# Performance work log

Measured on AMD Instinct MI355X. Metric: run time of the kernel, lower is better.

The kernel has to match this reference:

```python
import jax, jax.numpy as jnp
import numpy as np

B, L, DM = 2, 2048, 2048
DI = 2 * DM          # d_inner = expand * d_model
N = 16               # d_state
K = 4                # d_conv
R = DM // 16         # dt_rank = ceil(d_model/16) = 128
FF = 8192            # intermediate_size
EPS = 1e-5


def _silu(x):
    return x * jax.nn.sigmoid(x)


def _ln(x, w, b):
    mu = jnp.mean(x, -1, keepdims=True)
    var = jnp.mean((x - mu) ** 2, -1, keepdims=True)
    return (x - mu) * jax.lax.rsqrt(var + EPS) * w + b


def setup_inputs() -> dict:
    key = jax.random.key(0)
    ks = jax.random.split(key, 8)

    def w(k, shape, fan_in):
        return jax.random.normal(k, shape, jnp.float32) / np.sqrt(fan_in).astype(np.float32)

    return {
        "hidden_states": jax.random.normal(ks[0], (B, L, DM), jnp.float32),
        "ln1_w": jnp.ones((DM,), jnp.float32),
        "ln1_b": jnp.zeros((DM,), jnp.float32),
        "W_in": w(ks[1], (2 * DI, DM), DM),      # in_proj (x and gate merged)
        "conv_w": w(ks[2], (DI, K), K),           # depthwise causal conv weights
        "conv_b": jnp.zeros((DI,), jnp.float32),
        "W_x": w(ks[3], (R + 2 * N, DI), DI),     # x_proj -> [dt_rank | B | C]
        "W_dt": w(ks[4], (DI, R), R),             # dt_proj (bias applied in scan)
        "b_dt": jnp.full((DI,), -2.0, jnp.float32),
        "A": -jnp.tile(jnp.arange(1.0, N + 1.0, dtype=jnp.float32), (DI, 1)),  # (DI, N)
        "Dp": jnp.ones((DI,), jnp.float32),
        "W_out": w(ks[5], (DM, DI), DI),
        "ln2_w": jnp.ones((DM,), jnp.float32),
        "ln2_b": jnp.zeros((DM,), jnp.float32),
        "W_fc1": w(ks[6], (2 * FF, DM), DM),      # GLU: [gate | y]
        "W_fc2": w(ks[7], (DM, FF), FF),
    }


def reference(hidden_states, ln1_w, ln1_b, W_in, conv_w, conv_b, W_x, W_dt, b_dt,
              A, Dp, W_out, ln2_w, ln2_b, W_fc1, W_fc2):
    # --- input layernorm + Phi4Mamba (prefill path: causal_conv1d_fn + selective_scan_fn) ---
    res = hidden_states
    x = _ln(hidden_states, ln1_w, ln1_b)

    xz = jnp.einsum('bld,ed->ble', x, W_in)           # (B, L, 2*DI)
    xs, gate = jnp.split(xz, 2, axis=-1)              # each (B, L, DI)

    # depthwise causal conv1d (width K) fused with silu
    xp = jnp.pad(xs, ((0, 0), (K - 1, 0), (0, 0)))
    conv = conv_b
    for k in range(K):
        conv = conv + xp[:, k:k + L, :] * conv_w[:, k]
    xs = _silu(conv)                                  # (B, L, DI)

    ssm = jnp.einsum('bld,ed->ble', xs, W_x)          # (B, L, R+2N)
    dt, Bm, Cm = ssm[..., :R], ssm[..., R:R + N], ssm[..., R + N:]
    delta = jax.nn.softplus(jnp.einsum('blr,dr->bld', dt, W_dt) + b_dt)  # (B, L, DI)

    def step(h, inp):
        d_t, b_t, c_t, x_t = inp                       # (B,DI),(B,N),(B,N),(B,DI)
        h = jnp.exp(d_t[..., None] * A) * h + (d_t * x_t)[..., None] * b_t[:, None, :]
        return h, jnp.einsum('bdn,bn->bd', h, c_t)

    h0 = jnp.zeros((B, DI, N), xs.dtype)
    _, ys = jax.lax.scan(step, h0, (delta.transpose(1, 0, 2), Bm.transpose(1, 0, 2),
                                    Cm.transpose(1, 0, 2), xs.transpose(1, 0, 2)))
    y = ys.transpose(1, 0, 2) + Dp * xs               # (B, L, DI)
    y = y * _silu(gate)                                # selective_scan z-gating
    attn_out = jnp.einsum('bld,ed->ble', y, W_out)    # (B, L, DM)

    hs = res + attn_out

    # --- post layernorm + GLU MLP ---
    res2 = hs
    x2 = _ln(hs, ln2_w, ln2_b)
    gy = jnp.einsum('bld,ed->ble', x2, W_fc1)         # (B, L, 2*FF)
    g, yy = jnp.split(gy, 2, axis=-1)
    mlp = jnp.einsum('blf,df->bld', yy * _silu(g), W_fc2)
    return res2 + mlp
```

## Files before the change

### kernel.cpp

```cpp
#include <hip/hip_runtime.h>
#include <hip/hip_bf16.h>

typedef unsigned short u16;
typedef unsigned int u32;

#define L_SEQ 2048
#define DMODEL 2048
#define DINNER 4096
#define NSTATE 16
#define MROWS 4096
#define CHUNK 32
#define NCHK  64

typedef __bf16 bf16x8 __attribute__((ext_vector_type(8)));
typedef float f32x4 __attribute__((ext_vector_type(4)));

__device__ __forceinline__ u16 f2bf(float f) {
    union { float f; u32 u; } v; v.f = f;
    u32 u = v.u;
    u32 r = (u + 0x7fffu + ((u >> 16) & 1u)) >> 16;
    return (u16)r;
}
__device__ __forceinline__ float bf2f(u16 h) {
    union { u32 u; float f; } v; v.u = ((u32)h) << 16;
    return v.f;
}

__device__ __forceinline__ void gload16(const void* g, void* l) {
    __builtin_amdgcn_global_load_lds((const __attribute__((address_space(1))) void*)g,
                                     (__attribute__((address_space(3))) void*)l, 16, 0, 0);
}

__global__ __launch_bounds__(256) void cvt_kernel(const float* __restrict__ src,
                                                  u16* __restrict__ dst, long nsrc) {
    long i = ((long)blockIdx.x * 256 + threadIdx.x) * 8;
    union { uint4 v; u16 u[8]; } o;
    if (i < nsrc) {
        f32x4 a = *(const f32x4*)(src + i);
        f32x4 b = *(const f32x4*)(src + i + 4);
#pragma unroll
        for (int j = 0; j < 4; ++j) { o.u[j] = f2bf(a[j]); o.u[4 + j] = f2bf(b[j]); }
    } else {
#pragma unroll
        for (int j = 0; j < 8; ++j) o.u[j] = 0;
    }
    *(uint4*)(dst + i) = o.v;
}

__global__ __launch_bounds__(256) void ln_kernel(const float* __restrict__ in,
                                                 const float* __restrict__ w,
                                                 const float* __restrict__ b,
                                                 u16* __restrict__ out) {
    const long row = blockIdx.x;
    const float* x = in + row * DMODEL;
    const int t = threadIdx.x;
    f32x4 v0 = *(const f32x4*)(x + t * 8);
    f32x4 v1 = *(const f32x4*)(x + t * 8 + 4);
    float s = 0.f, sq = 0.f;
#pragma unroll
    for (int j = 0; j < 4; ++j) {
        s += v0[j] + v1[j];
        sq += v0[j] * v0[j] + v1[j] * v1[j];
    }
#pragma unroll
    for (int off = 32; off > 0; off >>= 1) {
        s += __shfl_down(s, off);
        sq += __shfl_down(sq, off);
    }
    __shared__ float red[8];
    __shared__ float stats[2];
    const int wid = t >> 6, lane = t & 63;
    if (lane == 0) { red[wid] = s; red[4 + wid] = sq; }
    __syncthreads();
    if (t == 0) {
        float S = red[0] + red[1] + red[2] + red[3];
        float Q = red[4] + red[5] + red[6] + red[7];
        float mu = S / (float)DMODEL;
        stats[0] = mu;
        stats[1] = rsqrtf(Q / (float)DMODEL - mu * mu + 1e-5f);
    }
    __syncthreads();
    float mu = stats[0], rstd = stats[1];
    union { uint4 v; u16 u[8]; } o;
#pragma unroll
    for (int j = 0; j < 8; ++j) {
        float xv = (j < 4) ? v0[j] : v1[j - 4];
        o.u[j] = f2bf((xv - mu) * rstd * w[t * 8 + j] + b[t * 8 + j]);
    }
    *(uint4*)(out + row * DMODEL + t * 8) = o.v;
}

__global__ __launch_bounds__(256) void reduce_ln_kernel(const float* __restrict__ p0,
                                                        const float* __restrict__ p1,
                                                        const float* __restrict__ add,
                                                        const float* __restrict__ w,
                                                        const float* __restrict__ b,
                                                        float* __restrict__ hs_out,
                                                        u16* __restrict__ ln_out) {
    const long row = blockIdx.x;
    const long base = row * DMODEL;
    const int t = threadIdx.x;
    f32x4 v0, v1;
    {
        f32x4 a0 = *(const f32x4*)(p0 + base + t * 8);
        f32x4 a1 = *(const f32x4*)(p0 + base + t * 8 + 4);
        f32x4 b0 = *(const f32x4*)(p1 + base + t * 8);
        f32x4 b1 = *(const f32x4*)(p1 + base + t * 8 + 4);
        f32x4 c0 = *(const f32x4*)(add + base + t * 8);
        f32x4 c1 = *(const f32x4*)(add + base + t * 8 + 4);
#pragma unroll
        for (int j = 0; j < 4; ++j) { v0[j] = a0[j] + b0[j] + c0[j]; v1[j] = a1[j] + b1[j] + c1[j]; }
    }
    *(f32x4*)(hs_out + base + t * 8) = v0;
    *(f32x4*)(hs_out + base + t * 8 + 4) = v1;
    float s = 0.f, sq = 0.f;
#pragma unroll
    for (int j = 0; j < 4; ++j) {
        s += v0[j] + v1[j];
        sq += v0[j] * v0[j] + v1[j] * v1[j];
    }
#pragma unroll
    for (int off = 32; off > 0; off >>= 1) {
        s += __shfl_down(s, off);
        sq += __shfl_down(sq, off);
    }
    __shared__ float red[8];
    __shared__ float stats[2];
    const int wid = t >> 6, lane = t & 63;
    if (lane == 0) { red[wid] = s; red[4 + wid] = sq; }
    __syncthreads();
    if (t == 0) {
        float S = red[0] + red[1] + red[2] + red[3];
        float Q = red[4] + red[5] + red[6] + red[7];
        float mu = S / (float)DMODEL;
        stats[0] = mu;
        stats[1] = rsqrtf(Q / (float)DMODEL - mu * mu + 1e-5f);
    }
    __syncthreads();
    float mu = stats[0], rstd = stats[1];
    union { uint4 v; u16 u[8]; } o;
#pragma unroll
    for (int j = 0; j < 8; ++j) {
        float xv = (j < 4) ? v0[j] : v1[j - 4];
        o.u[j] = f2bf((xv - mu) * rstd * w[t * 8 + j] + b[t * 8 + j]);
    }
    *(uint4*)(ln_out + base + t * 8) = o.v;
}

template <int MODE>
__global__ __launch_bounds__(256) void gemm_bt(const u16* __restrict__ A,
                                               const u16* __restrict__ W,
                                               float* __restrict__ Cf,
                                               u16* __restrict__ Cb,
                                               const float* __restrict__ addv,
                                               int M, int N, int K, int lda, int ldb) {
    __shared__ u16 As[128 * 64];
    __shared__ u16 Bs[128 * 64];
    const int tid = threadIdx.x;
    const int wid = tid >> 6;
    const int lane = tid & 63;
    const int m0 = blockIdx.y << 7;
    const int n0 = blockIdx.x << 7;
    const long koff = (long)blockIdx.z * K;
    const long zoff = (long)blockIdx.z * M * N;
    const int wr = (wid >> 1) << 6;
    const int wc = (wid & 1) << 6;
    const int l15 = lane & 15;
    const int lhi = lane >> 4;

    f32x4 acc[4][4];
#pragma unroll
    for (int i = 0; i < 4; ++i)
#pragma unroll
        for (int j = 0; j < 4; ++j) acc[i][j] = (f32x4){0.f, 0.f, 0.f, 0.f};

    const int srow = (wid << 3) + (lane >> 3);
    const int scol = (lane & 7) << 3;

    const u16* aBase = A + (long)(m0 + srow) * lda + scol + koff;
    const u16* bBase = W + (long)(n0 + srow) * (long)ldb + scol + koff;

    for (int k0 = 0; k0 < K; k0 += 64) {
#pragma unroll
        for (int i = 0; i < 4; ++i) {
            gload16(aBase + (long)(i * 32) * lda + k0, &As[((i << 5) + (wid << 3)) << 6]);
            gload16(bBase + (long)(i * 32) * ldb + k0, &Bs[((i << 5) + (wid << 3)) << 6]);
        }
        __syncthreads();
#pragma unroll
        for (int kk = 0; kk < 64; kk += 32) {
            bf16x8 af[4], bfr[4];
#pragma unroll
            for (int i = 0; i < 4; ++i)
                af[i] = *(const bf16x8*)&As[((wr + (i << 4) + l15) << 6) + kk + (lhi << 3)];
#pragma unroll
            for (int j = 0; j < 4; ++j)
                bfr[j] = *(const bf16x8*)&Bs[((wc + (j << 4) + l15) << 6) + kk + (lhi << 3)];
#pragma unroll
            for (int i = 0; i < 4; ++i)
#pragma unroll
                for (int j = 0; j < 4; ++j)
                    acc[i][j] = __builtin_amdgcn_mfma_f32_16x16x32_bf16(af[i], bfr[j], acc[i][j], 0, 0, 0);
        }
        __syncthreads();
    }

#pragma unroll
    for (int i = 0; i < 4; ++i) {
#pragma unroll
        for (int j = 0; j < 4; ++j) {
#pragma unroll
            for (int r = 0; r < 4; ++r) {
                int row = m0 + wr + (i << 4) + (lhi << 2) + r;
                int col = n0 + wc + (j << 4) + l15;
                long idx = (long)row * N + col;
                float v = acc[i][j][r];
                if (MODE == 2) v += addv[idx];
                if (MODE == 1) Cb[idx] = f2bf(v);
                else Cf[zoff + idx] = v;
            }
        }
    }
}

template <int MODE>
__global__ __launch_bounds__(512, 2) void gemm8(const u16* __restrict__ A,
                                                const u16* __restrict__ W,
                                                float* __restrict__ Cf,
                                                u16* __restrict__ Cb,
                                                const float* __restrict__ addv,
                                                int M, int N, int K, int lda, int ldb) {
    __shared__ u16 lds[4][2][256 * 32];
    const int tid = threadIdx.x;
    const int wid = tid >> 6;
    const int lane = tid & 63;
    const int wr = wid >> 2;
    const int wc = wid & 3;
    const int l15 = lane & 15;
    const int lhi = lane >> 4;
    const int sw = (l15 >> 1) & 3;
    const long koff = (long)blockIdx.z * K;
    const long zoff = (long)blockIdx.z * M * N;

    const int nwg = gridDim.x * gridDim.y;
    const int flat = blockIdx.y * gridDim.x + blockIdx.x;
    const int q8 = nwg >> 3, r8 = nwg & 7;
    const int xcd = flat & 7, lid = flat >> 3;
    const int swz = (xcd < r8 ? xcd * (q8 + 1) : r8 * (q8 + 1) + (xcd - r8) * q8) + lid;
    const int m0 = (swz % gridDim.y) << 8;
    const int n0 = (swz / gridDim.y) << 8;

    const int srow = lane >> 2;
    const int gc16 = (lane & 3) ^ ((lane >> 3) & 3);

    f32x4 acc[8][4];
#pragma unroll
    for (int i = 0; i < 8; ++i)
#pragma unroll
        for (int j = 0; j < 4; ++j) acc[i][j] = (f32x4){0.f, 0.f, 0.f, 0.f};

#define STAGE_A(t, j)                                                                              \
    gload16(A + (long)(m0 + (j) * 128 + wid * 16 + srow) * lda + koff + (long)(t) * 32 + gc16 * 8, \
            &lds[(t) & 3][0][((j) * 128 + wid * 16) * 32])
#define STAGE_B(t, j)                                                                              \
    gload16(W + (long)(n0 + (j) * 128 + wid * 16 + srow) * (long)ldb + koff + (long)(t) * 32 + gc16 * 8, \
            &lds[(t) & 3][1][((j) * 128 + wid * 16) * 32])

    STAGE_A(0, 0); STAGE_A(0, 1); STAGE_B(0, 0); STAGE_B(0, 1);
    STAGE_A(1, 0); STAGE_A(1, 1); STAGE_B(1, 0); STAGE_B(1, 1);
    STAGE_A(2, 0); STAGE_A(2, 1); STAGE_B(2, 0); STAGE_B(2, 1);
    asm volatile("s_waitcnt vmcnt(8)" ::: "memory");
    __builtin_amdgcn_s_barrier();
    __builtin_amdgcn_sched_barrier(0);

    const int nt = K >> 5;
    for (int t = 0; t < nt; ++t) {
        const u16* Ab = &lds[t & 3][0][0];
        const u16* Bb = &lds[t & 3][1][0];
        bf16x8 afrg[4], bfrg[4];
#pragma unroll
        for (int f = 0; f < 4; ++f)
            afrg[f] = *(const bf16x8*)&Ab[(wr * 128 + f * 16 + l15) * 32 + ((lhi ^ sw) << 3)];
#pragma unroll
        for (int f = 0; f < 4; ++f)
            bfrg[f] = *(const bf16x8*)&Bb[(wc * 64 + f * 16 + l15) * 32 + ((lhi ^ sw) << 3)];
        if (t + 3 < nt) { STAGE_A(t + 3, 0); STAGE_A(t + 3, 1); }
        __builtin_amdgcn_s_barrier();
        __builtin_amdgcn_s_setprio(1);
#pragma unroll
        for (int i = 0; i < 4; ++i)
#pragma unroll
            for (int j = 0; j < 4; ++j)
                acc[i][j] = __builtin_amdgcn_mfma_f32_16x16x32_bf16(afrg[i], bfrg[j], acc[i][j], 0, 0, 0);
        __builtin_amdgcn_s_setprio(0);
#pragma unroll
        for (int f = 0; f < 4; ++f)
            afrg[f] = *(const bf16x8*)&Ab[(wr * 128 + (f + 4) * 16 + l15) * 32 + ((lhi ^ sw) << 3)];
        if (t + 3 < nt) { STAGE_B(t + 3, 0); STAGE_B(t + 3, 1); }
        __builtin_amdgcn_s_barrier();
        __builtin_amdgcn_s_setprio(1);
#pragma unroll
        for (int i = 0; i < 4; ++i)
#pragma unroll
            for (int j = 0; j < 4; ++j)
                acc[i + 4][j] = __builtin_amdgcn_mfma_f32_16x16x32_bf16(afrg[i], bfrg[j], acc[i + 4][j], 0, 0, 0);
        __builtin_amdgcn_s_setprio(0);
        const int rem = nt - 2 - t;
        if (rem >= 2)      { asm volatile("s_waitcnt vmcnt(8)" ::: "memory"); }
        else if (rem == 1) { asm volatile("s_waitcnt vmcnt(4)" ::: "memory"); }
        else if (rem == 0) { asm volatile("s_waitcnt vmcnt(0)" ::: "memory"); }
        __builtin_amdgcn_s_barrier();
        __builtin_amdgcn_sched_barrier(0);
    }
#undef STAGE_A
#undef STAGE_B

#pragma unroll
    for (int i = 0; i < 8; ++i) {
#pragma unroll
        for (int j = 0; j < 4; ++j) {
#pragma unroll
            for (int r = 0; r < 4; ++r) {
                int row = m0 + wr * 128 + i * 16 + lhi * 4 + r;
                int col = n0 + wc * 64 + j * 16 + l15;
                long idx = (long)row * N + col;
                float v = acc[i][j][r];
                if (MODE == 2) v += addv[idx];
                if (MODE == 1) Cb[idx] = f2bf(v);
                else Cf[zoff + idx] = v;
            }
        }
    }
}

__global__ __launch_bounds__(256) void reduce_add_kernel(const float* __restrict__ p0,
                                                         const float* __restrict__ p1,
                                                         const float* __restrict__ add,
                                                         float* __restrict__ out) {
    long i = ((long)blockIdx.x * 256 + threadIdx.x) * 4;
    f32x4 a = *(const f32x4*)(p0 + i);
    f32x4 b = *(const f32x4*)(p1 + i);
    f32x4 c = *(const f32x4*)(add + i);
    f32x4 o;
#pragma unroll
    for (int j = 0; j < 4; ++j) o[j] = a[j] + b[j] + c[j];
    *(f32x4*)(out + i) = o;
}

__global__ __launch_bounds__(256) void reduce4_bf16_kernel(const float* __restrict__ p,
                                                           u16* __restrict__ outb) {
    long i = ((long)blockIdx.x * 256 + threadIdx.x) * 4;
    const long S = 4096L * 256;
    f32x4 a = *(const f32x4*)(p + i);
    f32x4 b = *(const f32x4*)(p + S + i);
    f32x4 c = *(const f32x4*)(p + 2 * S + i);
    f32x4 d = *(const f32x4*)(p + 3 * S + i);
    union { uint2 v; u16 u[4]; } o;
#pragma unroll
    for (int j = 0; j < 4; ++j) o.u[j] = f2bf(a[j] + b[j] + c[j] + d[j]);
    *(uint2*)(outb + i) = o.v;
}

__global__ __launch_bounds__(256) void conv_silu_kernel(const u16* __restrict__ xz,
                                                        const float* __restrict__ cw,
                                                        const float* __restrict__ cb,
                                                        u16* __restrict__ act_out) {
    const int d0 = (blockIdx.x * 256 + threadIdx.x) * 8;
    const int bl = blockIdx.y;
    const int l = bl & (L_SEQ - 1);
    float acc[8];
    float wt[8][4];
#pragma unroll
    for (int j = 0; j < 8; ++j) {
        f32x4 wj = *(const f32x4*)(cw + (d0 + j) * 4);
        wt[j][0] = wj[0]; wt[j][1] = wj[1]; wt[j][2] = wj[2]; wt[j][3] = wj[3];
        acc[j] = cb[d0 + j];
    }
#pragma unroll
    for (int k = 0; k < 4; ++k) {
        int ls = l + k - 3;
        if (ls >= 0) {
            union { uint4 v; u16 u[8]; } xv;
            xv.v = *(const uint4*)(xz + (long)(bl + k - 3) * (2 * DINNER) + d0);
#pragma unroll
            for (int j = 0; j < 8; ++j) acc[j] = fmaf(bf2f(xv.u[j]), wt[j][k], acc[j]);
        }
    }
    union { uint4 v; u16 u[8]; } ob;
#pragma unroll
    for (int j = 0; j < 8; ++j) {
        float c = acc[j];
        ob.u[j] = f2bf(c / (1.f + __expf(-c)));
    }
    *(uint4*)(act_out + (long)bl * DINNER + d0) = ob.v;
}

__global__ __launch_bounds__(256) void scan1_kernel(float* __restrict__ dpre,
                                                    const u16* __restrict__ xs,
                                                    const u16* __restrict__ ssmb,
                                                    const float* __restrict__ Am,
                                                    const float* __restrict__ bdt,
                                                    float* __restrict__ hend,
                                                    float* __restrict__ sumd) {
    const int d = blockIdx.x * 256 + threadIdx.x;
    const int c = blockIdx.y;
    const int b = blockIdx.z;
    float a2[NSTATE];
#pragma unroll
    for (int n = 0; n < NSTATE; ++n) a2[n] = Am[d * NSTATE + n] * 1.4426950408889634f;
    float h[NSTATE];
#pragma unroll
    for (int n = 0; n < NSTATE; ++n) h[n] = 0.f;
    const float bd = bdt[d];
    float sd = 0.f;
    const long base = (long)b * L_SEQ + (long)c * CHUNK;
    for (int i = 0; i < CHUNK; ++i) {
        const long row = base + i;
        float dpv = dpre[row * DINNER + d] + bd;
        float delta = (dpv > 20.f) ? dpv : log1pf(__expf(dpv));
        dpre[row * DINNER + d] = delta;
        sd += delta;
        float dx = delta * bf2f(xs[row * DINNER + d]);
        const u16* sb = ssmb + row * 256;
#pragma unroll
        for (int n = 0; n < NSTATE; ++n)
            h[n] = __builtin_amdgcn_exp2f(delta * a2[n]) * h[n] + dx * bf2f(sb[128 + n]);
    }
    float* hb = hend + ((long)(b * NCHK + c) * DINNER + d) * NSTATE;
#pragma unroll
    for (int n = 0; n < NSTATE; n += 4)
        *(f32x4*)(hb + n) = (f32x4){h[n], h[n + 1], h[n + 2], h[n + 3]};
    sumd[(long)(b * NCHK + c) * DINNER + d] = sd;
}

__global__ __launch_bounds__(256) void scan2_kernel(float* __restrict__ hend,
                                                    const float* __restrict__ sumd,
                                                    const float* __restrict__ Am) {
    const long idx = (long)blockIdx.x * 256 + threadIdx.x;
    const int n = (int)(idx & 15);
    const int d = (int)((idx >> 4) & (DINNER - 1));
    const int b = (int)(idx >> 16);
    const float a2 = Am[d * NSTATE + n] * 1.4426950408889634f;
    float carry = 0.f;
    for (int c = 0; c < NCHK; ++c) {
        const long soff = (long)(b * NCHK + c) * DINNER + d;
        const long hoff = soff * NSTATE + n;
        float he = hend[hoff];
        float P = __builtin_amdgcn_exp2f(a2 * sumd[soff]);
        hend[hoff] = carry;
        carry = he + P * carry;
    }
}

__global__ __launch_bounds__(256) void scan3_kernel(const float* __restrict__ delta_,
                                                    const u16* __restrict__ xs,
                                                    const u16* __restrict__ ssmb,
                                                    const u16* __restrict__ xz,
                                                    const float* __restrict__ Am,
                                                    const float* __restrict__ Dp,
                                                    const float* __restrict__ hinit,
                                                    u16* __restrict__ yb) {
    const int d = blockIdx.x * 256 + threadIdx.x;
    const int c = blockIdx.y;
    const int b = blockIdx.z;
    float a2[NSTATE];
#pragma unroll
    for (int n = 0; n < NSTATE; ++n) a2[n] = Am[d * NSTATE + n] * 1.4426950408889634f;
    float h[NSTATE];
    const float* hb = hinit + ((long)(b * NCHK + c) * DINNER + d) * NSTATE;
#pragma unroll
    for (int n = 0; n < NSTATE; n += 4) {
        f32x4 hv = *(const f32x4*)(hb + n);
        h[n] = hv[0]; h[n + 1] = hv[1]; h[n + 2] = hv[2]; h[n + 3] = hv[3];
    }
    const float dp = Dp[d];
    const long base = (long)b * L_SEQ + (long)c * CHUNK;
    for (int i = 0; i < CHUNK; ++i) {
        const long row = base + i;
        float delta = delta_[row * DINNER + d];
        float xt = bf2f(xs[row * DINNER + d]);
        float dx = delta * xt;
        const u16* sb = ssmb + row * 256;
        float y = 0.f;
#pragma unroll
        for (int n = 0; n < NSTATE; ++n) {
            float Bn = bf2f(sb[128 + n]);
            float Cn = bf2f(sb[144 + n]);
            h[n] = __builtin_amdgcn_exp2f(delta * a2[n]) * h[n] + dx * Bn;
            y = fmaf(h[n], Cn, y);
        }
        float g = bf2f(xz[row * (2 * DINNER) + DINNER + d]);
        float yv = (y + dp * xt) * (g / (1.f + __expf(-g)));
        yb[row * DINNER + d] = f2bf(yv);
    }
}

__global__ __launch_bounds__(256) void gated_act_kernel(const u16* __restrict__ gy,
                                                        u16* __restrict__ actb) {
    long i = ((long)blockIdx.x * 256 + threadIdx.x) * 8;
    long m = i >> 13;
    long f = i & 8191;
    const u16* gp = gy + m * 16384 + f;
    union { uint4 v; u16 u[8]; } gu, yu, ob;
    gu.v = *(const uint4*)gp;
    yu.v = *(const uint4*)(gp + 8192);
#pragma unroll
    for (int j = 0; j < 8; ++j) {
        float g = bf2f(gu.u[j]);
        float yv = bf2f(yu.u[j]);
        ob.u[j] = f2bf(yv * (g / (1.f + __expf(-g))));
    }
    *(uint4*)(actb + i) = ob.v;
}

extern "C" void kernel_launch(void* const* d_in, const int* in_sizes, int n_in,
                              void* d_out, int out_size, void* d_ws, size_t ws_size,
                              hipStream_t stream) {
    const float* hidden = (const float*)d_in[0];
    const float* ln1w   = (const float*)d_in[1];
    const float* ln1b   = (const float*)d_in[2];
    const float* W_in   = (const float*)d_in[3];
    const float* conv_w = (const float*)d_in[4];
    const float* conv_b = (const float*)d_in[5];
    const float* W_x    = (const float*)d_in[6];
    const float* W_dt   = (const float*)d_in[7];
    const float* b_dt   = (const float*)d_in[8];
    const float* Amat   = (const float*)d_in[9];
    const float* Dp     = (const float*)d_in[10];
    const float* W_out  = (const float*)d_in[11];
    const float* ln2w   = (const float*)d_in[12];
    const float* ln2b   = (const float*)d_in[13];
    const float* W_fc1  = (const float*)d_in[14];
    const float* W_fc2  = (const float*)d_in[15];
    float* out = (float*)d_out;

    char* ws = (char*)d_ws;
    const size_t SZ67 = 67108864;
    u16*   ACT   = (u16*)(ws);
    u16*   WB    = (u16*)(ws + SZ67);
    u16*   XZ    = (u16*)(ws + 2 * SZ67);
    float* DELTA = (float*)(ws + 4 * SZ67);
    u16*   SSMB  = (u16*)(ws + 5 * SZ67);
    float* HS    = (float*)(ws + 5 * SZ67 + 2097152);
    u16*   GY    = XZ;
    float* HEND  = (float*)WB;
    float* SUMD  = (float*)(ws + SZ67 + 33554432);
    float* PART2 = (float*)(ws + SZ67 + 37748736);
    float* PART  = DELTA;

    ln_kernel<<<MROWS, 256, 0, stream>>>(hidden, ln1w, ln1b, ACT);
    cvt_kernel<<<(int)((8192L * 2048) / 2048), 256, 0, stream>>>(W_in, WB, 8192L * 2048);
    gemm8<1><<<dim3(8192 / 256, MROWS / 256), 512, 0, stream>>>(ACT, WB, nullptr, XZ, nullptr,
                                                                MROWS, 8192, 2048, 2048, 2048);
    conv_silu_kernel<<<dim3(2, MROWS), 256, 0, stream>>>(XZ, conv_w, conv_b, ACT);
    cvt_kernel<<<(int)((256L * 4096) / 2048), 256, 0, stream>>>(W_x, WB, 160L * 4096);
    gemm_bt<0><<<dim3(2, 32, 4), 256, 0, stream>>>(ACT, WB, PART2, nullptr, nullptr,
                                                   MROWS, 256, 1024, 4096, 4096);
    reduce4_bf16_kernel<<<1024, 256, 0, stream>>>(PART2, SSMB);
    cvt_kernel<<<(int)((4096L * 128) / 2048), 256, 0, stream>>>(W_dt, WB, 4096L * 128);
    gemm8<0><<<dim3(4096 / 256, MROWS / 256), 512, 0, stream>>>(SSMB, WB, DELTA, nullptr, nullptr,
                                                                MROWS, 4096, 128, 256, 128);
    scan1_kernel<<<dim3(DINNER / 256, NCHK, 2), 256, 0, stream>>>(DELTA, ACT, SSMB, Amat, b_dt,
                                                                  HEND, SUMD);
    scan2_kernel<<<(2 * DINNER * NSTATE) / 256, 256, 0, stream>>>(HEND, SUMD, Amat);
    scan3_kernel<<<dim3(DINNER / 256, NCHK, 2), 256, 0, stream>>>(DELTA, ACT, SSMB, XZ, Amat, Dp,
                                                                  HEND, ACT);
    cvt_kernel<<<(int)((2048L * 4096) / 2048), 256, 0, stream>>>(W_out, WB, 2048L * 4096);
    gemm8<0><<<dim3(2048 / 256, MROWS / 256, 2), 512, 0, stream>>>(ACT, WB, PART, nullptr, nullptr,
                                                                   MROWS, 2048, 2048, 4096, 4096);
    reduce_ln_kernel<<<MROWS, 256, 0, stream>>>(PART, PART + 4096L * 2048, hidden,
                                                ln2w, ln2b, HS, ACT);
    cvt_kernel<<<(int)((16384L * 2048) / 2048), 256, 0, stream>>>(W_fc1, WB, 16384L * 2048);
    gemm8<1><<<dim3(16384 / 256, MROWS / 256), 512, 0, stream>>>(ACT, WB, nullptr, GY, nullptr,
                                                                 MROWS, 16384, 2048, 2048, 2048);
    gated_act_kernel<<<(int)((4096L * 8192) / 2048), 256, 0, stream>>>(GY, ACT);
    cvt_kernel<<<(int)((2048L * 8192) / 2048), 256, 0, stream>>>(W_fc2, WB, 2048L * 8192);
    gemm8<0><<<dim3(2048 / 256, MROWS / 256, 2), 512, 0, stream>>>(ACT, WB, PART, nullptr, nullptr,
                                                                   MROWS, 2048, 4096, 8192, 8192);
    reduce_add_kernel<<<(int)((4096L * 2048) / 1024), 256, 0, stream>>>(PART, PART + 4096L * 2048,
                                                                        HS, out);
}
```

Baseline: 1.057 ms.

## Fuse GLU activation into fc1 GEMM epilogue via interleaved weights; restructure gemm8 pipeline

The fc1 weight conversion now interleaves gate and value rows in groups of 16, so each GEMM tile holds matching gate/y columns. A new epilogue mode computes y*silu(g) in registers and writes the bf16 activation directly. This removes the separate gated-activation kernel and the write and re-read of the 4096x16384 intermediate. The gemm8 main loop is also reworked to prefetch 2 stages instead of 3 and process two k-tiles per iteration with fewer barriers. The shallower prefetch may expose more memory latency.

```diff
diff --git a/kernel.cpp b/kernel.cpp
--- a/kernel.cpp
+++ b/kernel.cpp
@@ -45,6 +45,22 @@
         for (int j = 0; j < 8; ++j) o.u[j] = 0;
     }
     *(uint4*)(dst + i) = o.v;
+}
+
+__global__ __launch_bounds__(256) void cvt_fc1_kernel(const float* __restrict__ src,
+                                                      u16* __restrict__ dst) {
+    long id = (long)blockIdx.x * 256 + threadIdx.x;
+    int r = (int)(id >> 8);
+    int c8 = (int)(id & 255) * 8;
+    int g16 = r >> 5, k = r & 31;
+    int sr = (k < 16) ? (g16 * 16 + k) : (8192 + g16 * 16 + (k - 16));
+    const float* s = src + (long)sr * 2048 + c8;
+    f32x4 a = *(const f32x4*)s;
+    f32x4 b = *(const f32x4*)(s + 4);
+    union { uint4 v; u16 u[8]; } o;
+#pragma unroll
+    for (int j = 0; j < 4; ++j) { o.u[j] = f2bf(a[j]); o.u[4 + j] = f2bf(b[j]); }
+    *(uint4*)(dst + (long)r * 2048 + c8) = o.v;
 }
 
 __global__ __launch_bounds__(256) void ln_kernel(const float* __restrict__ in,
@@ -215,7 +231,6 @@
                 int col = n0 + wc + (j << 4) + l15;
                 long idx = (long)row * N + col;
                 float v = acc[i][j][r];
-                if (MODE == 2) v += addv[idx];
                 if (MODE == 1) Cb[idx] = f2bf(v);
                 else Cf[zoff + idx] = v;
             }
@@ -228,7 +243,6 @@
                                                 const u16* __restrict__ W,
                                                 float* __restrict__ Cf,
                                                 u16* __restrict__ Cb,
-                                                const float* __restrict__ addv,
                                                 int M, int N, int K, int lda, int ldb) {
     __shared__ u16 lds[4][2][256 * 32];
     const int tid = threadIdx.x;
@@ -265,69 +279,94 @@
 #define STAGE_B(t, j)                                                                              \
     gload16(W + (long)(n0 + (j) * 128 + wid * 16 + srow) * (long)ldb + koff + (long)(t) * 32 + gc16 * 8, \
             &lds[(t) & 3][1][((j) * 128 + wid * 16) * 32])
+#define RD_A(buf, f0)  *(const bf16x8*)&lds[buf][0][((wr * 128 + (f0) * 16 + l15)) * 32 + ((lhi ^ sw) << 3)]
+#define RD_B(buf, f0)  *(const bf16x8*)&lds[buf][1][((wc * 64 + (f0) * 16 + l15)) * 32 + ((lhi ^ sw) << 3)]
+#define MFMA16(ab)                                                                                  \
+    __builtin_amdgcn_s_setprio(1);                                                                  \
+    _Pragma("unroll")                                                                               \
+    for (int ii = 0; ii < 4; ++ii)                                                                  \
+        _Pragma("unroll")                                                                           \
+        for (int jj = 0; jj < 4; ++jj)                                                              \
+            acc[(ab) + ii][jj] = __builtin_amdgcn_mfma_f32_16x16x32_bf16(a[ii], bb[jj], acc[(ab) + ii][jj], 0, 0, 0); \
+    __builtin_amdgcn_s_setprio(0);
 
     STAGE_A(0, 0); STAGE_A(0, 1); STAGE_B(0, 0); STAGE_B(0, 1);
     STAGE_A(1, 0); STAGE_A(1, 1); STAGE_B(1, 0); STAGE_B(1, 1);
-    STAGE_A(2, 0); STAGE_A(2, 1); STAGE_B(2, 0); STAGE_B(2, 1);
-    asm volatile("s_waitcnt vmcnt(8)" ::: "memory");
+    asm volatile("s_waitcnt vmcnt(4)" ::: "memory");
     __builtin_amdgcn_s_barrier();
     __builtin_amdgcn_sched_barrier(0);
 
-    const int nt = K >> 5;
-    for (int t = 0; t < nt; ++t) {
-        const u16* Ab = &lds[t & 3][0][0];
-        const u16* Bb = &lds[t & 3][1][0];
-        bf16x8 afrg[4], bfrg[4];
-#pragma unroll
-        for (int f = 0; f < 4; ++f)
-            afrg[f] = *(const bf16x8*)&Ab[(wr * 128 + f * 16 + l15) * 32 + ((lhi ^ sw) << 3)];
-#pragma unroll
-        for (int f = 0; f < 4; ++f)
-            bfrg[f] = *(const bf16x8*)&Bb[(wc * 64 + f * 16 + l15) * 32 + ((lhi ^ sw) << 3)];
-        if (t + 3 < nt) { STAGE_A(t + 3, 0); STAGE_A(t + 3, 1); }
-        __builtin_amdgcn_s_barrier();
-        __builtin_amdgcn_s_setprio(1);
-#pragma unroll
-        for (int i = 0; i < 4; ++i)
-#pragma unroll
-            for (int j = 0; j < 4; ++j)
-                acc[i][j] = __builtin_amdgcn_mfma_f32_16x16x32_bf16(afrg[i], bfrg[j], acc[i][j], 0, 0, 0);
-        __builtin_amdgcn_s_setprio(0);
-#pragma unroll
-        for (int f = 0; f < 4; ++f)
-            afrg[f] = *(const bf16x8*)&Ab[(wr * 128 + (f + 4) * 16 + l15) * 32 + ((lhi ^ sw) << 3)];
-        if (t + 3 < nt) { STAGE_B(t + 3, 0); STAGE_B(t + 3, 1); }
-        __builtin_amdgcn_s_barrier();
-        __builtin_amdgcn_s_setprio(1);
-#pragma unroll
-        for (int i = 0; i < 4; ++i)
-#pragma unroll
-            for (int j = 0; j < 4; ++j)
-                acc[i + 4][j] = __builtin_amdgcn_mfma_f32_16x16x32_bf16(afrg[i], bfrg[j], acc[i + 4][j], 0, 0, 0);
-        __builtin_amdgcn_s_setprio(0);
-        const int rem = nt - 2 - t;
-        if (rem >= 2)      { asm volatile("s_waitcnt vmcnt(8)" ::: "memory"); }
-        else if (rem == 1) { asm volatile("s_waitcnt vmcnt(4)" ::: "memory"); }
-        else if (rem == 0) { asm volatile("s_waitcnt vmcnt(0)" ::: "memory"); }
+    const int nt2 = K >> 6;
+    for (int i = 0; i < nt2; ++i) {
+        const int t0 = 2 * i;
+        const int b0 = t0 & 3, b1 = (t0 + 1) & 3;
+        const bool more = (i + 1 < nt2);
+        bf16x8 a[4], bb[4];
+#pragma unroll
+        for (int f = 0; f < 4; ++f) a[f] = RD_A(b0, f);
+#pragma unroll
+        for (int f = 0; f < 4; ++f) bb[f] = RD_B(b0, f);
+        if (more) { STAGE_A(t0 + 2, 0); STAGE_A(t0 + 2, 1); }
+        MFMA16(0)
+#pragma unroll
+        for (int f = 0; f < 4; ++f) a[f] = RD_A(b0, f + 4);
+        if (more) { STAGE_B(t0 + 2, 0); STAGE_B(t0 + 2, 1); }
+        MFMA16(4)
+        if (more) { asm volatile("s_waitcnt vmcnt(4)" ::: "memory"); }
+        else      { asm volatile("s_waitcnt vmcnt(0)" ::: "memory"); }
         __builtin_amdgcn_s_barrier();
         __builtin_amdgcn_sched_barrier(0);
+#pragma unroll
+        for (int f = 0; f < 4; ++f) a[f] = RD_A(b1, f);
+#pragma unroll
+        for (int f = 0; f < 4; ++f) bb[f] = RD_B(b1, f);
+        if (more) { STAGE_A(t0 + 3, 0); STAGE_A(t0 + 3, 1); }
+        MFMA16(0)
+#pragma unroll
+        for (int f = 0; f < 4; ++f) a[f] = RD_A(b1, f + 4);
+        if (more) { STAGE_B(t0 + 3, 0); STAGE_B(t0 + 3, 1); }
+        MFMA16(4)
+        if (more) {
+            asm volatile("s_waitcnt vmcnt(4)" ::: "memory");
+            __builtin_amdgcn_s_barrier();
+            __builtin_amdgcn_sched_barrier(0);
+        }
     }
 #undef STAGE_A
 #undef STAGE_B
-
-#pragma unroll
-    for (int i = 0; i < 8; ++i) {
-#pragma unroll
-        for (int j = 0; j < 4; ++j) {
-#pragma unroll
-            for (int r = 0; r < 4; ++r) {
-                int row = m0 + wr * 128 + i * 16 + lhi * 4 + r;
-                int col = n0 + wc * 64 + j * 16 + l15;
-                long idx = (long)row * N + col;
-                float v = acc[i][j][r];
-                if (MODE == 2) v += addv[idx];
-                if (MODE == 1) Cb[idx] = f2bf(v);
-                else Cf[zoff + idx] = v;
+#undef RD_A
+#undef RD_B
+#undef MFMA16
+
+    if (MODE == 3) {
+#pragma unroll
+        for (int i = 0; i < 8; ++i) {
+#pragma unroll
+            for (int jp = 0; jp < 2; ++jp) {
+                const int j = 2 * jp;
+#pragma unroll
+                for (int r = 0; r < 4; ++r) {
+                    int row = m0 + wr * 128 + i * 16 + lhi * 4 + r;
+                    int f = ((n0 + wc * 64) >> 1) + jp * 16 + l15;
+                    float g = acc[i][j][r];
+                    float yv = acc[i][j + 1][r];
+                    Cb[(long)row * (N >> 1) + f] = f2bf(yv * (g / (1.f + __expf(-g))));
+                }
+            }
+        }
+    } else {
+#pragma unroll
+        for (int i = 0; i < 8; ++i) {
+#pragma unroll
+            for (int j = 0; j < 4; ++j) {
+#pragma unroll
+                for (int r = 0; r < 4; ++r) {
+                    int row = m0 + wr * 128 + i * 16 + lhi * 4 + r;
+                    int col = n0 + wc * 64 + j * 16 + l15;
+                    long idx = (long)row * N + col;
+                    if (MODE == 1) Cb[idx] = f2bf(acc[i][j][r]);
+                    else Cf[zoff + idx] = acc[i][j][r];
+                }
             }
         }
     }
@@ -493,24 +532,6 @@
         float yv = (y + dp * xt) * (g / (1.f + __expf(-g)));
         yb[row * DINNER + d] = f2bf(yv);
     }
-}
-
-__global__ __launch_bounds__(256) void gated_act_kernel(const u16* __restrict__ gy,
-                                                        u16* __restrict__ actb) {
-    long i = ((long)blockIdx.x * 256 + threadIdx.x) * 8;
-    long m = i >> 13;
-    long f = i & 8191;
-    const u16* gp = gy + m * 16384 + f;
-    union { uint4 v; u16 u[8]; } gu, yu, ob;
-    gu.v = *(const uint4*)gp;
-    yu.v = *(const uint4*)(gp + 8192);
-#pragma unroll
-    for (int j = 0; j < 8; ++j) {
-        float g = bf2f(gu.u[j]);
-        float yv = bf2f(yu.u[j]);
-        ob.u[j] = f2bf(yv * (g / (1.f + __expf(-g))));
-    }
-    *(uint4*)(actb + i) = ob.v;
 }
 
 extern "C" void kernel_launch(void* const* d_in, const int* in_sizes, int n_in,
@@ -542,7 +563,6 @@
     float* DELTA = (float*)(ws + 4 * SZ67);
     u16*   SSMB  = (u16*)(ws + 5 * SZ67);
     float* HS    = (float*)(ws + 5 * SZ67 + 2097152);
-    u16*   GY    = XZ;
     float* HEND  = (float*)WB;
     float* SUMD  = (float*)(ws + SZ67 + 33554432);
     float* PART2 = (float*)(ws + SZ67 + 37748736);
@@ -550,7 +570,7 @@
 
     ln_kernel<<<MROWS, 256, 0, stream>>>(hidden, ln1w, ln1b, ACT);
     cvt_kernel<<<(int)((8192L * 2048) / 2048), 256, 0, stream>>>(W_in, WB, 8192L * 2048);
-    gemm8<1><<<dim3(8192 / 256, MROWS / 256), 512, 0, stream>>>(ACT, WB, nullptr, XZ, nullptr,
+    gemm8<1><<<dim3(8192 / 256, MROWS / 256), 512, 0, stream>>>(ACT, WB, nullptr, XZ,
                                                                 MROWS, 8192, 2048, 2048, 2048);
     conv_silu_kernel<<<dim3(2, MROWS), 256, 0, stream>>>(XZ, conv_w, conv_b, ACT);
     cvt_kernel<<<(int)((256L * 4096) / 2048), 256, 0, stream>>>(W_x, WB, 160L * 4096);
@@ -558,7 +578,7 @@
                                                    MROWS, 256, 1024, 4096, 4096);
     reduce4_bf16_kernel<<<1024, 256, 0, stream>>>(PART2, SSMB);
     cvt_kernel<<<(int)((4096L * 128) / 2048), 256, 0, stream>>>(W_dt, WB, 4096L * 128);
-    gemm8<0><<<dim3(4096 / 256, MROWS / 256), 512, 0, stream>>>(SSMB, WB, DELTA, nullptr, nullptr,
+    gemm8<0><<<dim3(4096 / 256, MROWS / 256), 512, 0, stream>>>(SSMB, WB, DELTA, nullptr,
                                                                 MROWS, 4096, 128, 256, 128);
     scan1_kernel<<<dim3(DINNER / 256, NCHK, 2), 256, 0, stream>>>(DELTA, ACT, SSMB, Amat, b_dt,
                                                                   HEND, SUMD);
@@ -566,16 +586,15 @@
     scan3_kernel<<<dim3(DINNER / 256, NCHK, 2), 256, 0, stream>>>(DELTA, ACT, SSMB, XZ, Amat, Dp,
                                                                   HEND, ACT);
     cvt_kernel<<<(int)((2048L * 4096) / 2048), 256, 0, stream>>>(W_out, WB, 2048L * 4096);
-    gemm8<0><<<dim3(2048 / 256, MROWS / 256, 2), 512, 0, stream>>>(ACT, WB, PART, nullptr, nullptr,
+    gemm8<0><<<dim3(2048 / 256, MROWS / 256, 2), 512, 0, stream>>>(ACT, WB, PART, nullptr,
                                                                    MROWS, 2048, 2048, 4096, 4096);
     reduce_ln_kernel<<<MROWS, 256, 0, stream>>>(PART, PART + 4096L * 2048, hidden,
                                                 ln2w, ln2b, HS, ACT);
-    cvt_kernel<<<(int)((16384L * 2048) / 2048), 256, 0, stream>>>(W_fc1, WB, 16384L * 2048);
-    gemm8<1><<<dim3(16384 / 256, MROWS / 256), 512, 0, stream>>>(ACT, WB, nullptr, GY, nullptr,
+    cvt_fc1_kernel<<<16384, 256, 0, stream>>>(W_fc1, WB);
+    gemm8<3><<<dim3(16384 / 256, MROWS / 256), 512, 0, stream>>>(ACT, WB, nullptr, XZ,
                                                                  MROWS, 16384, 2048, 2048, 2048);
-    gated_act_kernel<<<(int)((4096L * 8192) / 2048), 256, 0, stream>>>(GY, ACT);
     cvt_kernel<<<(int)((2048L * 8192) / 2048), 256, 0, stream>>>(W_fc2, WB, 2048L * 8192);
-    gemm8<0><<<dim3(2048 / 256, MROWS / 256, 2), 512, 0, stream>>>(ACT, WB, PART, nullptr, nullptr,
+    gemm8<0><<<dim3(2048 / 256, MROWS / 256, 2), 512, 0, stream>>>(XZ, WB, PART, nullptr,
                                                                    MROWS, 2048, 4096, 8192, 8192);
     reduce_add_kernel<<<(int)((4096L * 2048) / 1024), 256, 0, stream>>>(PART, PART + 4096L * 2048,
                                                                         HS, out);
```

Result: faster. 1.001 ms (-5.3%).
